# Optimization experiments

Measured on AMD Instinct MI355X. Metric: run time of the kernel, lower is better.

Reference implementation:

```python
import jax, jax.numpy as jnp
import numpy as np

B, NZ, L = 8, 16, 512
E, DM, NH, HD = 256, 512, 16, 32
FF, NL, E1D, PDIM, PMAX = 1024, 8, 32, 64, 24
EPS_LN = 1e-5
EPS_D = 1e-12


def _ln(x, g, b):
    m = jnp.mean(x, axis=-1, keepdims=True)
    v = jnp.mean((x - m) ** 2, axis=-1, keepdims=True)
    return (x - m) / jnp.sqrt(v + EPS_LN) * g + b


def setup_inputs() -> dict:
    key = jax.random.key(0)
    ks = iter(jax.random.split(key, 32))
    rn = lambda shape, fan: jax.random.normal(next(ks), shape, jnp.float32) / np.float32(np.sqrt(fan))
    inp = {
        "z": jax.random.normal(next(ks), (B, NZ, L), jnp.float32),
        "x": jax.random.uniform(next(ks), (B, 20, L), jnp.float32),
        # embeddings
        "pos_table": rn((2 * PMAX + 1, PDIM), 1.0),
        "aa_table": rn((20, E1D), 1.0),
        # embed_x: Linear(nz,E), relu, Linear(E,E)
        "ex_w1": rn((NZ, E), NZ), "ex_b1": jnp.zeros((E,), jnp.float32),
        "ex_w2": rn((E, E), E), "ex_b2": jnp.zeros((E,), jnp.float32),
        # per-layer stacked params
        "Wq": rn((NL, E, DM), E), "Wk": rn((NL, E, DM), E), "Wv": rn((NL, E, DM), E),
        "Wo": rn((NL, DM, E), DM), "bo": jnp.zeros((NL, E), jnp.float32),
        "W2d": rn((NL, PDIM, NH), PDIM), "b2d": jnp.zeros((NL, NH), jnp.float32),
        "W1": rn((NL, E + E1D, FF), E + E1D), "b1": jnp.zeros((NL, FF), jnp.float32),
        "W2": rn((NL, FF, E), FF), "b2": jnp.zeros((NL, E), jnp.float32),
        "g1": jnp.ones((NL, E), jnp.float32), "be1": jnp.zeros((NL, E), jnp.float32),
        "g2": jnp.ones((NL, E), jnp.float32), "be2": jnp.zeros((NL, E), jnp.float32),
        # mlp_3d: Linear(E,E), relu, Linear(E,3)
        "m3_w1": rn((E, E), E), "m3_b1": jnp.zeros((E,), jnp.float32),
        "m3_w2": rn((E, 3), E), "m3_b2": jnp.zeros((3,), jnp.float32),
    }
    return inp


def reference(z, x, pos_table, aa_table, ex_w1, ex_b1, ex_w2, ex_b2,
              Wq, Wk, Wv, Wo, bo, W2d, b2d, W1, b1, W2, b2,
              g1, be1, g2, be2, m3_w1, m3_b1, m3_w2, m3_b2):
    Bn, _, Ln = z.shape
    h = jnp.transpose(z, (0, 2, 1))  # (B, L, nz)
    # relative-position bins: argmin over integer bins == clip to [-PMAX, PMAX]
    rel = jnp.arange(Ln)[None, :] - jnp.arange(Ln)[:, None]
    bins = jnp.clip(rel, -PMAX, PMAX) + PMAX
    pe = pos_table[bins]  # (L, L, PDIM), batch-replicated
    e_aa = aa_table[jnp.argmax(x, axis=1)]  # (B, L, E1D)
    # embed_x MLP
    h = jax.nn.relu(h @ ex_w1 + ex_b1) @ ex_w2 + ex_b2  # (B, L, E)
    scale = np.float32(1.0 / np.sqrt(DM))  # dp_attn_norm='d_model'
    for i in range(NL):
        q = (h @ Wq[i]).reshape(Bn, Ln, NH, HD) * scale
        k = (h @ Wk[i]).reshape(Bn, Ln, NH, HD)
        v = (h @ Wv[i]).reshape(Bn, Ln, NH, HD)
        # learned pairwise bias: mlp_2d then transpose(1,3).transpose(2,3) -> bias[h,i,j] = out[i,j,h]
        bias = jnp.einsum('lmp,ph->hlm', pe, W2d[i]) + b2d[i][:, None, None]
        scores = jnp.einsum('blhd,bmhd->bhlm', q, k) + bias[None]
        attn = jax.nn.softmax(scores, axis=-1)
        o = jnp.einsum('bhlm,bmhd->blhd', attn, v).reshape(Bn, Ln, DM)
        h = _ln(h + (o @ Wo[i] + bo[i]), g1[i], be1[i])
        um = jnp.concatenate([h, e_aa], axis=-1)  # (B, L, E+E1D)
        s2 = jax.nn.relu(um @ W1[i] + b1[i]) @ W2[i] + b2[i]
        h = _ln(h + s2, g2[i], be2[i])
    r = jax.nn.relu(h @ m3_w1 + m3_b1) @ m3_w2 + m3_b2  # (B, L, 3)
    # distance map (get_coords=False path)
    d = jnp.sqrt(jnp.sum((r[:, None, :, :] - r[:, :, None, :]) ** 2, axis=-1) + EPS_D)
    return d  # (B, L, L)
```

## Files before the change

### kernel.cpp

```cpp
#include <hip/hip_runtime.h>
#include <math.h>

constexpr int Bn = 8, NZ = 16, Ln = 512;
constexpr int E = 256, DM = 512, NH = 16, HD = 32;
constexpr int FF = 1024, NL = 8, E1D = 32, PDIM = 64, PMAX = 24;
constexpr int ROWS = Bn * Ln;
constexpr float QSCALE = 0.04419417382415922f;

typedef __attribute__((ext_vector_type(8))) short bf16x8;
typedef __attribute__((ext_vector_type(4))) float floatx4;

__device__ inline unsigned short f2b(float f) {
  union { float f; unsigned u; } v; v.f = f;
  unsigned r = (v.u + 0x7FFF + ((v.u >> 16) & 1)) >> 16;
  return (unsigned short)r;
}
__device__ inline float b2f(unsigned short u) {
  union { unsigned u; float f; } v; v.u = ((unsigned)u) << 16; return v.f;
}

__device__ inline void gll16(const void* g, void* l) {
  __builtin_amdgcn_global_load_lds(
      (const __attribute__((address_space(1))) void*)g,
      (__attribute__((address_space(3))) void*)l, 16, 0, 0);
}

__global__ __launch_bounds__(256) void transpose_qkv(
    const float* __restrict__ Wq, const float* __restrict__ Wk,
    const float* __restrict__ Wv, unsigned short* __restrict__ qkvT)
{
  __shared__ float t[32][33];
  int zb = blockIdx.z;
  int which = zb / NL, l = zb % NL;
  const float* s = (which == 0 ? Wq : which == 1 ? Wk : Wv) + (size_t)l * E * DM;
  unsigned short* d = qkvT + (size_t)l * 3 * DM * E + (size_t)which * DM * E;
  int c0 = blockIdx.x * 32, r0 = blockIdx.y * 32;
  int tx = threadIdx.x & 31, ty = threadIdx.x >> 5;
  #pragma unroll
  for (int i = 0; i < 4; ++i)
    t[ty + i * 8][tx] = s[(size_t)(r0 + ty + i * 8) * DM + c0 + tx];
  __syncthreads();
  #pragma unroll
  for (int i = 0; i < 4; ++i)
    d[(size_t)(c0 + ty + i * 8) * E + r0 + tx] = f2b(t[tx][ty + i * 8]);
}

__global__ __launch_bounds__(256) void transpose_bf16(
    const float* __restrict__ src, unsigned short* __restrict__ dst,
    int R, int C, size_t sls, size_t dls)
{
  __shared__ float t[32][33];
  int l = blockIdx.z;
  int c0 = blockIdx.x * 32, r0 = blockIdx.y * 32;
  int tx = threadIdx.x & 31, ty = threadIdx.x >> 5;
  const float* s = src + (size_t)l * sls;
  unsigned short* d = dst + (size_t)l * dls;
  #pragma unroll
  for (int i = 0; i < 4; ++i)
    t[ty + i * 8][tx] = s[(size_t)(r0 + ty + i * 8) * C + c0 + tx];
  __syncthreads();
  #pragma unroll
  for (int i = 0; i < 4; ++i)
    d[(size_t)(c0 + ty + i * 8) * R + r0 + tx] = f2b(t[tx][ty + i * 8]);
}

__global__ __launch_bounds__(256) void embed1_kernel(
    const float* __restrict__ z, const float* __restrict__ x,
    const float* __restrict__ aa,
    const float* __restrict__ w1, const float* __restrict__ b1,
    float* __restrict__ t0, unsigned short* __restrict__ umb)
{
  int row = blockIdx.x;
  int b = row >> 9, l = row & (Ln - 1);
  int t = threadIdx.x;
  __shared__ float zs[NZ];
  __shared__ int am_s;
  if (t < NZ) zs[t] = z[((size_t)b * NZ + t) * Ln + l];
  if (t == 0) {
    const float* xp = x + (size_t)b * 20 * Ln + l;
    int am = 0; float bv = xp[0];
    for (int c = 1; c < 20; ++c) { float vv = xp[(size_t)c * Ln]; if (vv > bv) { bv = vv; am = c; } }
    am_s = am;
  }
  __syncthreads();
  float a1 = b1[t];
  #pragma unroll
  for (int nz = 0; nz < NZ; ++nz) a1 += zs[nz] * w1[nz * E + t];
  t0[(size_t)row * E + t] = fmaxf(a1, 0.f);
  if (t < E1D) umb[(size_t)row * (E + E1D) + E + t] = f2b(aa[am_s * E1D + t]);
}

__global__ __launch_bounds__(256) void bias_kernel(
    const float* __restrict__ pos, const float* __restrict__ W2d,
    const float* __restrict__ b2d, float* __restrict__ bias49)
{
  int layer = blockIdx.x;
  for (int idx = threadIdx.x; idx < NH * 49; idx += 256) {
    int hh = idx / 49, bin = idx % 49;
    float acc = b2d[layer * NH + hh];
    for (int p = 0; p < PDIM; ++p)
      acc += pos[bin * PDIM + p] * W2d[((size_t)layer * PDIM + p) * NH + hh];
    bias49[(size_t)layer * NH * 49 + hh * 49 + bin] = acc;
  }
}

template<int BM, int BN, bool BIAS, bool RELU, bool OUTBF16, bool QKV>
__global__ __launch_bounds__(256) void gemm_mfma(
    const unsigned short* __restrict__ A, const unsigned short* __restrict__ Bt,
    const float* __restrict__ bias,
    float* __restrict__ Cf, unsigned short* __restrict__ Cb, int N, int K)
{
  constexpr int MT = BM / 32, NT = BN / 32;
  __shared__ __align__(16) unsigned short As[BM][32];
  __shared__ __align__(16) unsigned short Bs[BN][32];
  const int tid = threadIdx.x;
  const int wave = tid >> 6, ln = tid & 63;
  const int quad = ln >> 4, l16 = ln & 15;
  const int wm = wave >> 1, wn = wave & 1;
  const int m0 = blockIdx.y * BM, n0 = blockIdx.x * BN;

  const int lrow = ln >> 2, chunk = ln & 3;
  const int schunk = chunk ^ ((lrow >> 1) & 3);
  const unsigned short* aSrc = A + (size_t)(m0 + wave * 16 + lrow) * K + schunk * 8;
  const unsigned short* bSrc = Bt + (size_t)(n0 + wave * 16 + lrow) * K + schunk * 8;
  const int rkey = (l16 >> 1) & 3;

  floatx4 acc[MT][NT] = {};

  for (int kb = 0; kb < K; kb += 32) {
    __syncthreads();
    #pragma unroll
    for (int it = 0; it < BM / 64; ++it)
      gll16(aSrc + (size_t)it * 64 * K + kb, &As[it * 64 + wave * 16][0]);
    #pragma unroll
    for (int it = 0; it < BN / 64; ++it)
      gll16(bSrc + (size_t)it * 64 * K + kb, &Bs[it * 64 + wave * 16][0]);
    __syncthreads();
    bf16x8 af[MT], bfr[NT];
    #pragma unroll
    for (int i = 0; i < MT; ++i)
      af[i] = *(const bf16x8*)&As[wm * (BM / 2) + i * 16 + l16][(quad ^ rkey) * 8];
    #pragma unroll
    for (int j = 0; j < NT; ++j)
      bfr[j] = *(const bf16x8*)&Bs[wn * (BN / 2) + j * 16 + l16][(quad ^ rkey) * 8];
    #pragma unroll
    for (int i = 0; i < MT; ++i)
      #pragma unroll
      for (int j = 0; j < NT; ++j)
        acc[i][j] = __builtin_amdgcn_mfma_f32_16x16x32_bf16(af[i], bfr[j], acc[i][j], 0, 0, 0);
  }

  #pragma unroll
  for (int i = 0; i < MT; ++i)
    #pragma unroll
    for (int j = 0; j < NT; ++j) {
      int col = n0 + wn * (BN / 2) + j * 16 + l16;
      float bv = BIAS ? bias[col] : 0.f;
      float sc = QKV ? (col < 512 ? QSCALE : 1.f) : 1.f;
      #pragma unroll
      for (int r = 0; r < 4; ++r) {
        int rowg = m0 + wm * (BM / 2) + i * 16 + quad * 4 + r;
        float v = acc[i][j][r] * sc + bv;
        if (RELU) v = fmaxf(v, 0.f);
        if (OUTBF16) Cb[(size_t)rowg * N + col] = f2b(v);
        else Cf[(size_t)rowg * N + col] = v;
      }
    }
}

__global__ __launch_bounds__(256) void gemm_n256(
    const unsigned short* __restrict__ A, const unsigned short* __restrict__ Bt,
    const float* __restrict__ bias, const float* __restrict__ resid,
    float* __restrict__ Cf, int K)
{
  __shared__ __align__(16) unsigned short As[32][64];
  __shared__ __align__(16) unsigned short Bs[32][64];
  const int tid = threadIdx.x;
  const int wave = tid >> 6, ln = tid & 63;
  const int quad = ln >> 4, l16 = ln & 15;
  const int wm = wave >> 1, wn = wave & 1;
  const int m0 = blockIdx.y * 32, n0 = blockIdx.x * 32;

  const int lrow = ln >> 3, chunk = ln & 7;
  const int schunk = chunk ^ lrow;
  const unsigned short* ap = A + (size_t)(m0 + wave * 8 + lrow) * K + schunk * 8;
  const unsigned short* bp = Bt + (size_t)(n0 + wave * 8 + lrow) * K + schunk * 8;
  const int rkey = l16 & 7;

  floatx4 acc = {};

  for (int kb = 0; kb < K; kb += 64) {
    __syncthreads();
    gll16(ap + kb, &As[wave * 8][0]);
    gll16(bp + kb, &Bs[wave * 8][0]);
    __syncthreads();
    #pragma unroll
    for (int kc = 0; kc < 2; ++kc) {
      bf16x8 af = *(const bf16x8*)&As[wm * 16 + l16][((kc * 4 + quad) ^ rkey) * 8];
      bf16x8 bf = *(const bf16x8*)&Bs[wn * 16 + l16][((kc * 4 + quad) ^ rkey) * 8];
      acc = __builtin_amdgcn_mfma_f32_16x16x32_bf16(af, bf, acc, 0, 0, 0);
    }
  }

  const int col = n0 + wn * 16 + l16;
  const float bv = bias[col];
  #pragma unroll
  for (int r = 0; r < 4; ++r) {
    int rowg = m0 + wm * 16 + quad * 4 + r;
    Cf[(size_t)rowg * 256 + col] = acc[r] + bv + resid[(size_t)rowg * 256 + col];
  }
}

__global__ __launch_bounds__(256) void attn_kernel(
    const unsigned short* __restrict__ qkv, const float* __restrict__ bias49,
    unsigned short* __restrict__ o)
{
  const int i0 = blockIdx.x * 64;
  const int bh = blockIdx.y;
  const int b = bh >> 4, hh = bh & 15;
  const int tid = threadIdx.x;
  const int wave = tid >> 6, ln = tid & 63;
  const int quad = ln >> 4, l16 = ln & 15;

  __shared__ __align__(16) unsigned short Kt[64][40];
  __shared__ __align__(16) unsigned short Vt[32][72];
  __shared__ __align__(16) unsigned short Pw[4][2][16][72];
  __shared__ float bsh[49];

  if (tid < 49) bsh[tid] = bias49[hh * 49 + tid];

  const unsigned short* qkvb = qkv + (size_t)b * Ln * 1536;

  const int qrow = i0 + wave * 16 + l16;
  const bf16x8 qf = *(const bf16x8*)(qkvb + (size_t)qrow * 1536 + hh * 32 + quad * 8);

  float m[4], l[4];
  #pragma unroll
  for (int r = 0; r < 4; ++r) { m[r] = -1e30f; l[r] = 0.f; }
  floatx4 acc_o[2] = {};

  const int krow = tid >> 2, kch = (tid & 3) * 8;
  const int vkey = tid & 63, vch = (tid >> 6) * 8;

  for (int jt = 0; jt < 8; ++jt) {
    const int j0 = jt * 64;
    __syncthreads();
    *(float4*)&Kt[krow][kch] =
        *(const float4*)(qkvb + (size_t)(j0 + krow) * 1536 + 512 + hh * 32 + kch);
    bf16x8 vv = *(const bf16x8*)(qkvb + (size_t)(j0 + vkey) * 1536 + 1024 + hh * 32 + vch);
    #pragma unroll
    for (int i = 0; i < 8; ++i) Vt[vch + i][vkey] = (unsigned short)vv[i];
    __syncthreads();

    floatx4 s4[4];
    #pragma unroll
    for (int t = 0; t < 4; ++t) {
      bf16x8 kf = *(const bf16x8*)&Kt[16 * t + l16][quad * 8];
      s4[t] = __builtin_amdgcn_mfma_f32_16x16x32_bf16(qf, kf, (floatx4){0.f, 0.f, 0.f, 0.f}, 0, 0, 0);
    }
    const int relmin = j0 - (i0 + 63), relmax = j0 + 63 - i0;
    if (relmin >= PMAX) {
      float bc = bsh[48];
      #pragma unroll
      for (int t = 0; t < 4; ++t)
        #pragma unroll
        for (int r = 0; r < 4; ++r) s4[t][r] += bc;
    } else if (relmax <= -PMAX) {
      float bc = bsh[0];
      #pragma unroll
      for (int t = 0; t < 4; ++t)
        #pragma unroll
        for (int r = 0; r < 4; ++r) s4[t][r] += bc;
    } else {
      const int base_rel = (j0 + l16) - (i0 + wave * 16 + quad * 4);
      #pragma unroll
      for (int t = 0; t < 4; ++t)
        #pragma unroll
        for (int r = 0; r < 4; ++r) {
          int rel = base_rel + 16 * t - r;
          rel = rel < -PMAX ? -PMAX : (rel > PMAX ? PMAX : rel);
          s4[t][r] += bsh[rel + PMAX];
        }
    }

    float mloc[4], alpha[4], psum[4];
    #pragma unroll
    for (int r = 0; r < 4; ++r) {
      mloc[r] = fmaxf(fmaxf(s4[0][r], s4[1][r]), fmaxf(s4[2][r], s4[3][r]));
      #pragma unroll
      for (int off = 1; off < 16; off <<= 1)
        mloc[r] = fmaxf(mloc[r], __shfl_xor(mloc[r], off, 64));
      float mnew = fmaxf(m[r], mloc[r]);
      alpha[r] = __expf(m[r] - mnew);
      m[r] = mnew;
      psum[r] = 0.f;
    }
    #pragma unroll
    for (int t = 0; t < 4; ++t)
      #pragma unroll
      for (int r = 0; r < 4; ++r) {
        float p = __expf(s4[t][r] - m[r]);
        s4[t][r] = p;
        psum[r] += p;
      }
    #pragma unroll
    for (int r = 0; r < 4; ++r) {
      #pragma unroll
      for (int off = 1; off < 16; off <<= 1)
        psum[r] += __shfl_xor(psum[r], off, 64);
      l[r] = l[r] * alpha[r] + psum[r];
      acc_o[0][r] *= alpha[r];
      acc_o[1][r] *= alpha[r];
    }

    #pragma unroll
    for (int t = 0; t < 4; ++t)
      #pragma unroll
      for (int r = 0; r < 4; ++r) {
        float p = s4[t][r];
        unsigned short hi = f2b(p);
        unsigned short lo = f2b(p - b2f(hi));
        Pw[wave][0][quad * 4 + r][16 * t + l16] = hi;
        Pw[wave][1][quad * 4 + r][16 * t + l16] = lo;
      }

    #pragma unroll
    for (int kh = 0; kh < 2; ++kh) {
      bf16x8 phi = *(const bf16x8*)&Pw[wave][0][l16][kh * 32 + quad * 8];
      bf16x8 plo = *(const bf16x8*)&Pw[wave][1][l16][kh * 32 + quad * 8];
      #pragma unroll
      for (int nt = 0; nt < 2; ++nt) {
        bf16x8 vf = *(const bf16x8*)&Vt[nt * 16 + l16][kh * 32 + quad * 8];
        acc_o[nt] = __builtin_amdgcn_mfma_f32_16x16x32_bf16(phi, vf, acc_o[nt], 0, 0, 0);
        acc_o[nt] = __builtin_amdgcn_mfma_f32_16x16x32_bf16(plo, vf, acc_o[nt], 0, 0, 0);
      }
    }
  }

  #pragma unroll
  for (int r = 0; r < 4; ++r) {
    float inv = 1.f / l[r];
    size_t rowg = (size_t)b * Ln + i0 + wave * 16 + quad * 4 + r;
    #pragma unroll
    for (int nt = 0; nt < 2; ++nt)
      o[rowg * 512 + hh * 32 + nt * 16 + l16] = f2b(acc_o[nt][r] * inv);
  }
}

__global__ __launch_bounds__(256) void ln_kernel(
    const float* __restrict__ xin, const float* __restrict__ g,
    const float* __restrict__ be, float* __restrict__ hout,
    unsigned short* __restrict__ bout, int bstride)
{
  const int w = threadIdx.x >> 6, lane = threadIdx.x & 63;
  const size_t row = (size_t)blockIdx.x * 4 + w;
  const int c0 = lane * 4;
  float4 v = *(const float4*)(xin + row * E + c0);
  float s = v.x + v.y + v.z + v.w;
  float s2 = v.x * v.x + v.y * v.y + v.z * v.z + v.w * v.w;
  #pragma unroll
  for (int off = 1; off < 64; off <<= 1) {
    s += __shfl_xor(s, off, 64);
    s2 += __shfl_xor(s2, off, 64);
  }
  const float mean = s * (1.f / E);
  const float rstd = rsqrtf(s2 * (1.f / E) - mean * mean + 1e-5f);
  const float4 gv = *(const float4*)(g + c0);
  const float4 bv = *(const float4*)(be + c0);
  float4 y;
  y.x = (v.x - mean) * rstd * gv.x + bv.x;
  y.y = (v.y - mean) * rstd * gv.y + bv.y;
  y.z = (v.z - mean) * rstd * gv.z + bv.z;
  y.w = (v.w - mean) * rstd * gv.w + bv.w;
  *(float4*)(hout + row * E + c0) = y;
  ushort4 yb;
  yb.x = f2b(y.x); yb.y = f2b(y.y); yb.z = f2b(y.z); yb.w = f2b(y.w);
  *(ushort4*)(bout + row * (size_t)bstride + c0) = yb;
}

template<bool RELU, bool BIAS, bool MIRROR>
__global__ __launch_bounds__(256) void gemm64f(
    const float* __restrict__ A, const float* __restrict__ B,
    const float* __restrict__ bias, float* __restrict__ C,
    unsigned short* __restrict__ mir, int N, int K)
{
  __shared__ __align__(16) float As[16][64];
  __shared__ __align__(16) float Bss[16][68];
  const int tid = threadIdx.x;
  const int tx = tid & 15, ty = tid >> 4;
  const int m0 = blockIdx.y * 64, n0 = blockIdx.x * 64;
  const int arow = tid >> 2, acol = (tid & 3) * 4;
  const int brow = tid >> 6, bcol = tid & 63;
  float acc[4][4] = {};
  for (int kb = 0; kb < K; kb += 16) {
    __syncthreads();
    float4 av = *(const float4*)(A + (size_t)(m0 + arow) * K + kb + acol);
    As[acol + 0][arow] = av.x; As[acol + 1][arow] = av.y;
    As[acol + 2][arow] = av.z; As[acol + 3][arow] = av.w;
    #pragma unroll
    for (int kk = 0; kk < 4; ++kk)
      Bss[brow + kk * 4][bcol] = B[(size_t)(kb + brow + kk * 4) * N + n0 + bcol];
    __syncthreads();
    #pragma unroll
    for (int k = 0; k < 16; ++k) {
      float4 a = *(const float4*)&As[k][4 * ty];
      float4 b = *(const float4*)&Bss[k][4 * tx];
      float av4[4] = {a.x, a.y, a.z, a.w};
      float bv4[4] = {b.x, b.y, b.z, b.w};
      #pragma unroll
      for (int ii = 0; ii < 4; ++ii)
        #pragma unroll
        for (int jj = 0; jj < 4; ++jj)
          acc[ii][jj] += av4[ii] * bv4[jj];
    }
  }
  #pragma unroll
  for (int ii = 0; ii < 4; ++ii) {
    size_t row = (size_t)m0 + 4 * ty + ii;
    int col = n0 + 4 * tx;
    float4 vv;
    vv.x = acc[ii][0]; vv.y = acc[ii][1]; vv.z = acc[ii][2]; vv.w = acc[ii][3];
    if (BIAS) {
      float4 bb = *(const float4*)(bias + col);
      vv.x += bb.x; vv.y += bb.y; vv.z += bb.z; vv.w += bb.w;
    }
    if (RELU) {
      vv.x = fmaxf(vv.x, 0.f); vv.y = fmaxf(vv.y, 0.f);
      vv.z = fmaxf(vv.z, 0.f); vv.w = fmaxf(vv.w, 0.f);
    }
    *(float4*)(C + row * N + col) = vv;
    if (MIRROR) {
      ushort4 mv;
      mv.x = f2b(vv.x); mv.y = f2b(vv.y); mv.z = f2b(vv.z); mv.w = f2b(vv.w);
      *(ushort4*)(mir + row * N + col) = mv;
    }
  }
}

__global__ __launch_bounds__(256) void final_r_kernel(
    const float* __restrict__ t1, const float* __restrict__ w2,
    const float* __restrict__ b2, float* __restrict__ r)
{
  int row = blockIdx.x, t = threadIdx.x;
  float xv = t1[(size_t)row * E + t];
  float p0 = xv * w2[t * 3 + 0];
  float p1 = xv * w2[t * 3 + 1];
  float p2 = xv * w2[t * 3 + 2];
  #pragma unroll
  for (int off = 32; off > 0; off >>= 1) {
    p0 += __shfl_down(p0, off, 64);
    p1 += __shfl_down(p1, off, 64);
    p2 += __shfl_down(p2, off, 64);
  }
  __shared__ float red[4][3];
  if ((t & 63) == 0) { int w = t >> 6; red[w][0] = p0; red[w][1] = p1; red[w][2] = p2; }
  __syncthreads();
  if (t < 3)
    r[(size_t)row * 3 + t] = red[0][t] + red[1][t] + red[2][t] + red[3][t] + b2[t];
}

__global__ __launch_bounds__(512) void dist_kernel(
    const float* __restrict__ r, float* __restrict__ out)
{
  int bi = blockIdx.x;
  int j = threadIdx.x;
  int b = bi >> 9;
  float x0 = r[(size_t)bi * 3 + 0];
  float y0 = r[(size_t)bi * 3 + 1];
  float z0 = r[(size_t)bi * 3 + 2];
  const float* rj = r + ((size_t)b * Ln + j) * 3;
  float dx = rj[0] - x0, dy = rj[1] - y0, dz = rj[2] - z0;
  out[(size_t)bi * Ln + j] = sqrtf(dx * dx + dy * dy + dz * dz + 1e-12f);
}

extern "C" void kernel_launch(void* const* d_in, const int* in_sizes, int n_in,
                              void* d_out, int out_size, void* d_ws, size_t ws_size,
                              hipStream_t stream)
{
  const float* z     = (const float*)d_in[0];
  const float* x     = (const float*)d_in[1];
  const float* pos   = (const float*)d_in[2];
  const float* aa    = (const float*)d_in[3];
  const float* ex_w1 = (const float*)d_in[4];
  const float* ex_b1 = (const float*)d_in[5];
  const float* ex_w2 = (const float*)d_in[6];
  const float* ex_b2 = (const float*)d_in[7];
  const float* Wq    = (const float*)d_in[8];
  const float* Wk    = (const float*)d_in[9];
  const float* Wv    = (const float*)d_in[10];
  const float* Wo    = (const float*)d_in[11];
  const float* bo    = (const float*)d_in[12];
  const float* W2d   = (const float*)d_in[13];
  const float* b2d   = (const float*)d_in[14];
  const float* W1    = (const float*)d_in[15];
  const float* b1    = (const float*)d_in[16];
  const float* W2    = (const float*)d_in[17];
  const float* b2    = (const float*)d_in[18];
  const float* g1    = (const float*)d_in[19];
  const float* be1   = (const float*)d_in[20];
  const float* g2    = (const float*)d_in[21];
  const float* be2   = (const float*)d_in[22];
  const float* m3w1  = (const float*)d_in[23];
  const float* m3b1  = (const float*)d_in[24];
  const float* m3w2  = (const float*)d_in[25];
  const float* m3b2  = (const float*)d_in[26];

  float* ws     = (float*)d_ws;
  float* h      = ws;
  float* t0     = h + (size_t)ROWS * E;
  float* r      = t0 + (size_t)ROWS * E;
  float* bias49 = r + (size_t)ROWS * 3;
  unsigned short* us = (unsigned short*)(bias49 + NL * NH * 49);
  unsigned short* hb   = us;
  unsigned short* umb  = hb  + (size_t)ROWS * E;
  unsigned short* qkvb = umb + (size_t)ROWS * (E + E1D);
  unsigned short* ob   = qkvb + (size_t)ROWS * 3 * DM;
  unsigned short* t1b  = ob  + (size_t)ROWS * DM;
  unsigned short* qkvT = t1b + (size_t)ROWS * FF;
  unsigned short* WoT  = qkvT + (size_t)NL * 3 * DM * E;
  unsigned short* W1T  = WoT  + (size_t)NL * E * DM;
  unsigned short* W2T  = W1T  + (size_t)NL * FF * (E+E1D);
  float* tmp = t0;
  float* t1f = (float*)t1b;

  transpose_qkv<<<dim3(DM/32, E/32, 3*NL), 256, 0, stream>>>(Wq, Wk, Wv, qkvT);
  transpose_bf16<<<dim3(E/32, DM/32, NL), 256, 0, stream>>>(
      Wo, WoT, DM, E, (size_t)DM * E, (size_t)DM * E);
  transpose_bf16<<<dim3(FF/32, (E+E1D)/32, NL), 256, 0, stream>>>(
      W1, W1T, E + E1D, FF, (size_t)(E+E1D) * FF, (size_t)(E+E1D) * FF);
  transpose_bf16<<<dim3(E/32, FF/32, NL), 256, 0, stream>>>(
      W2, W2T, FF, E, (size_t)FF * E, (size_t)FF * E);

  embed1_kernel<<<ROWS, 256, 0, stream>>>(z, x, aa, ex_w1, ex_b1, t0, umb);
  gemm64f<false,true,true><<<dim3(E/64, ROWS/64), 256, 0, stream>>>(
      t0, ex_w2, ex_b2, h, hb, E, E);
  bias_kernel<<<NL, 256, 0, stream>>>(pos, W2d, b2d, bias49);

  for (int i = 0; i < NL; ++i) {
    gemm_mfma<64,128,false,false,true,true><<<dim3(12, 64), 256, 0, stream>>>(
        hb, qkvT + (size_t)i * 3 * DM * E, nullptr, nullptr, qkvb, 3 * DM, E);
    attn_kernel<<<dim3(Ln/64, Bn*NH), 256, 0, stream>>>(
        qkvb, bias49 + (size_t)i * NH * 49, ob);
    gemm_n256<<<dim3(E/32, ROWS/32), 256, 0, stream>>>(
        ob, WoT + (size_t)i * DM * E, bo + (size_t)i * E, h, tmp, DM);
    ln_kernel<<<ROWS/4, 256, 0, stream>>>(tmp, g1 + (size_t)i * E, be1 + (size_t)i * E, h, umb, E + E1D);
    gemm_mfma<64,64,true,true,true,false><<<dim3(FF/64, ROWS/64), 256, 0, stream>>>(
        umb, W1T + (size_t)i * FF * (E+E1D), b1 + (size_t)i * FF, nullptr, t1b, FF, E + E1D);
    gemm_n256<<<dim3(E/32, ROWS/32), 256, 0, stream>>>(
        t1b, W2T + (size_t)i * E * FF, b2 + (size_t)i * E, h, tmp, FF);
    ln_kernel<<<ROWS/4, 256, 0, stream>>>(tmp, g2 + (size_t)i * E, be2 + (size_t)i * E, h, hb, E);
  }

  gemm64f<true,true,false><<<dim3(E/64, ROWS/64), 256, 0, stream>>>(
      h, m3w1, m3b1, t1f, nullptr, E, E);
  final_r_kernel<<<ROWS, 256, 0, stream>>>(t1f, m3w2, m3b2, r);
  dist_kernel<<<ROWS, 512, 0, stream>>>(r, (float*)d_out);
}
```

Before: 841.9 us.

## Fuse output-projection GEMMs with residual LayerNorm and use BK=64 for QKV

Replaces the N=256 GEMM plus separate LayerNorm kernel pair with a single gemm_ln kernel. Each block computes a full 16x256 row tile, adds bias and residual in shared memory, and applies LayerNorm before writing fp32 h and the bf16 copy. This removes a launch and an fp32 intermediate round-trip per LN, but each block now reloads the whole 256-column weight slice and the grid shrinks to 256 blocks. The QKV GEMM also gets a BK=64 K-loop variant to halve the barrier count per K step.

New measurement: 822.8 us. 1.02x faster.

```diff
diff --git a/kernel.cpp b/kernel.cpp
--- a/kernel.cpp
+++ b/kernel.cpp
@@ -104,50 +104,83 @@
   }
 }
 
-template<int BM, int BN, bool BIAS, bool RELU, bool OUTBF16, bool QKV>
+template<int BM, int BN, int BK, bool BIAS, bool RELU, bool OUTBF16, bool QKV>
 __global__ __launch_bounds__(256) void gemm_mfma(
     const unsigned short* __restrict__ A, const unsigned short* __restrict__ Bt,
     const float* __restrict__ bias,
     float* __restrict__ Cf, unsigned short* __restrict__ Cb, int N, int K)
 {
   constexpr int MT = BM / 32, NT = BN / 32;
-  __shared__ __align__(16) unsigned short As[BM][32];
-  __shared__ __align__(16) unsigned short Bs[BN][32];
+  __shared__ __align__(16) unsigned short As[BM][BK];
+  __shared__ __align__(16) unsigned short Bs[BN][BK];
   const int tid = threadIdx.x;
   const int wave = tid >> 6, ln = tid & 63;
   const int quad = ln >> 4, l16 = ln & 15;
   const int wm = wave >> 1, wn = wave & 1;
   const int m0 = blockIdx.y * BM, n0 = blockIdx.x * BN;
 
-  const int lrow = ln >> 2, chunk = ln & 3;
-  const int schunk = chunk ^ ((lrow >> 1) & 3);
-  const unsigned short* aSrc = A + (size_t)(m0 + wave * 16 + lrow) * K + schunk * 8;
-  const unsigned short* bSrc = Bt + (size_t)(n0 + wave * 16 + lrow) * K + schunk * 8;
-  const int rkey = (l16 >> 1) & 3;
-
   floatx4 acc[MT][NT] = {};
 
-  for (int kb = 0; kb < K; kb += 32) {
-    __syncthreads();
-    #pragma unroll
-    for (int it = 0; it < BM / 64; ++it)
-      gll16(aSrc + (size_t)it * 64 * K + kb, &As[it * 64 + wave * 16][0]);
-    #pragma unroll
-    for (int it = 0; it < BN / 64; ++it)
-      gll16(bSrc + (size_t)it * 64 * K + kb, &Bs[it * 64 + wave * 16][0]);
-    __syncthreads();
-    bf16x8 af[MT], bfr[NT];
-    #pragma unroll
-    for (int i = 0; i < MT; ++i)
-      af[i] = *(const bf16x8*)&As[wm * (BM / 2) + i * 16 + l16][(quad ^ rkey) * 8];
-    #pragma unroll
-    for (int j = 0; j < NT; ++j)
-      bfr[j] = *(const bf16x8*)&Bs[wn * (BN / 2) + j * 16 + l16][(quad ^ rkey) * 8];
-    #pragma unroll
-    for (int i = 0; i < MT; ++i)
+  if constexpr (BK == 32) {
+    const int lrow = ln >> 2, chunk = ln & 3;
+    const int schunk = chunk ^ ((lrow >> 1) & 3);
+    const unsigned short* aSrc = A + (size_t)(m0 + wave * 16 + lrow) * K + schunk * 8;
+    const unsigned short* bSrc = Bt + (size_t)(n0 + wave * 16 + lrow) * K + schunk * 8;
+    const int rkey = (l16 >> 1) & 3;
+
+    for (int kb = 0; kb < K; kb += 32) {
+      __syncthreads();
+      #pragma unroll
+      for (int it = 0; it < BM / 64; ++it)
+        gll16(aSrc + (size_t)it * 64 * K + kb, &As[it * 64 + wave * 16][0]);
+      #pragma unroll
+      for (int it = 0; it < BN / 64; ++it)
+        gll16(bSrc + (size_t)it * 64 * K + kb, &Bs[it * 64 + wave * 16][0]);
+      __syncthreads();
+      bf16x8 af[MT], bfr[NT];
+      #pragma unroll
+      for (int i = 0; i < MT; ++i)
+        af[i] = *(const bf16x8*)&As[wm * (BM / 2) + i * 16 + l16][(quad ^ rkey) * 8];
       #pragma unroll
       for (int j = 0; j < NT; ++j)
-        acc[i][j] = __builtin_amdgcn_mfma_f32_16x16x32_bf16(af[i], bfr[j], acc[i][j], 0, 0, 0);
+        bfr[j] = *(const bf16x8*)&Bs[wn * (BN / 2) + j * 16 + l16][(quad ^ rkey) * 8];
+      #pragma unroll
+      for (int i = 0; i < MT; ++i)
+        #pragma unroll
+        for (int j = 0; j < NT; ++j)
+          acc[i][j] = __builtin_amdgcn_mfma_f32_16x16x32_bf16(af[i], bfr[j], acc[i][j], 0, 0, 0);
+    }
+  } else {
+    const int lrow = ln >> 3, chunk = ln & 7;
+    const int schunk = chunk ^ lrow;
+    const unsigned short* aSrc = A + (size_t)(m0 + wave * 8 + lrow) * K + schunk * 8;
+    const unsigned short* bSrc = Bt + (size_t)(n0 + wave * 8 + lrow) * K + schunk * 8;
+
+    for (int kb = 0; kb < K; kb += 64) {
+      __syncthreads();
+      #pragma unroll
+      for (int it = 0; it < BM / 32; ++it)
+        gll16(aSrc + (size_t)(it * 32) * K + kb, &As[it * 32 + wave * 8][0]);
+      #pragma unroll
+      for (int it = 0; it < BN / 32; ++it)
+        gll16(bSrc + (size_t)(it * 32) * K + kb, &Bs[it * 32 + wave * 8][0]);
+      __syncthreads();
+      #pragma unroll
+      for (int kc = 0; kc < 2; ++kc) {
+        bf16x8 af[MT], bfr[NT];
+        #pragma unroll
+        for (int i = 0; i < MT; ++i)
+          af[i] = *(const bf16x8*)&As[wm * (BM / 2) + i * 16 + l16][(((kc * 4 + quad) ^ (l16 & 7)) * 8)];
+        #pragma unroll
+        for (int j = 0; j < NT; ++j)
+          bfr[j] = *(const bf16x8*)&Bs[wn * (BN / 2) + j * 16 + l16][(((kc * 4 + quad) ^ (l16 & 7)) * 8)];
+        #pragma unroll
+        for (int i = 0; i < MT; ++i)
+          #pragma unroll
+          for (int j = 0; j < NT; ++j)
+            acc[i][j] = __builtin_amdgcn_mfma_f32_16x16x32_bf16(af[i], bfr[j], acc[i][j], 0, 0, 0);
+      }
+    }
   }
 
   #pragma unroll
@@ -168,46 +201,82 @@
     }
 }
 
-__global__ __launch_bounds__(256) void gemm_n256(
+__global__ __launch_bounds__(256) void gemm_ln(
     const unsigned short* __restrict__ A, const unsigned short* __restrict__ Bt,
-    const float* __restrict__ bias, const float* __restrict__ resid,
-    float* __restrict__ Cf, int K)
-{
-  __shared__ __align__(16) unsigned short As[32][64];
-  __shared__ __align__(16) unsigned short Bs[32][64];
+    const float* __restrict__ bias, float* __restrict__ h,
+    const float* __restrict__ g, const float* __restrict__ be,
+    unsigned short* __restrict__ outb, int bstride, int K)
+{
+  __shared__ __align__(16) unsigned short As[16][64];
+  __shared__ __align__(16) unsigned short Bs[256][64];
+  __shared__ __align__(16) float vtile[16][260];
   const int tid = threadIdx.x;
-  const int wave = tid >> 6, ln = tid & 63;
+  const int w = tid >> 6, ln = tid & 63;
   const int quad = ln >> 4, l16 = ln & 15;
-  const int wm = wave >> 1, wn = wave & 1;
-  const int m0 = blockIdx.y * 32, n0 = blockIdx.x * 32;
-
+  const int m0 = blockIdx.x * 16;
   const int lrow = ln >> 3, chunk = ln & 7;
   const int schunk = chunk ^ lrow;
-  const unsigned short* ap = A + (size_t)(m0 + wave * 8 + lrow) * K + schunk * 8;
-  const unsigned short* bp = Bt + (size_t)(n0 + wave * 8 + lrow) * K + schunk * 8;
-  const int rkey = l16 & 7;
-
-  floatx4 acc = {};
+  const unsigned short* aSrc = A + (size_t)(m0 + w * 8 + lrow) * K + schunk * 8;
+  const unsigned short* bSrc = Bt + (size_t)(w * 8 + lrow) * K + schunk * 8;
+
+  floatx4 acc[4] = {};
 
   for (int kb = 0; kb < K; kb += 64) {
     __syncthreads();
-    gll16(ap + kb, &As[wave * 8][0]);
-    gll16(bp + kb, &Bs[wave * 8][0]);
+    if (w < 2) gll16(aSrc + kb, &As[w * 8][0]);
+    #pragma unroll
+    for (int it = 0; it < 8; ++it)
+      gll16(bSrc + (size_t)(it * 32) * K + kb, &Bs[it * 32 + w * 8][0]);
     __syncthreads();
     #pragma unroll
     for (int kc = 0; kc < 2; ++kc) {
-      bf16x8 af = *(const bf16x8*)&As[wm * 16 + l16][((kc * 4 + quad) ^ rkey) * 8];
-      bf16x8 bf = *(const bf16x8*)&Bs[wn * 16 + l16][((kc * 4 + quad) ^ rkey) * 8];
-      acc = __builtin_amdgcn_mfma_f32_16x16x32_bf16(af, bf, acc, 0, 0, 0);
-    }
-  }
-
-  const int col = n0 + wn * 16 + l16;
-  const float bv = bias[col];
-  #pragma unroll
-  for (int r = 0; r < 4; ++r) {
-    int rowg = m0 + wm * 16 + quad * 4 + r;
-    Cf[(size_t)rowg * 256 + col] = acc[r] + bv + resid[(size_t)rowg * 256 + col];
+      bf16x8 af = *(const bf16x8*)&As[l16][(((kc * 4 + quad) ^ (l16 & 7)) * 8)];
+      #pragma unroll
+      for (int nt = 0; nt < 4; ++nt) {
+        bf16x8 bf = *(const bf16x8*)&Bs[w * 64 + nt * 16 + l16][(((kc * 4 + quad) ^ (l16 & 7)) * 8)];
+        acc[nt] = __builtin_amdgcn_mfma_f32_16x16x32_bf16(af, bf, acc[nt], 0, 0, 0);
+      }
+    }
+  }
+
+  #pragma unroll
+  for (int nt = 0; nt < 4; ++nt) {
+    int col = w * 64 + nt * 16 + l16;
+    float bv = bias[col];
+    #pragma unroll
+    for (int r = 0; r < 4; ++r) {
+      int row = quad * 4 + r;
+      vtile[row][col] = acc[nt][r] + bv + h[(size_t)(m0 + row) * E + col];
+    }
+  }
+  __syncthreads();
+
+  const int c0 = ln * 4;
+  #pragma unroll
+  for (int rr = 0; rr < 4; ++rr) {
+    const int lr = w * 4 + rr;
+    float4 v = *(const float4*)&vtile[lr][c0];
+    float s = v.x + v.y + v.z + v.w;
+    float s2 = v.x * v.x + v.y * v.y + v.z * v.z + v.w * v.w;
+    #pragma unroll
+    for (int off = 1; off < 64; off <<= 1) {
+      s += __shfl_xor(s, off, 64);
+      s2 += __shfl_xor(s2, off, 64);
+    }
+    const float mean = s * (1.f / E);
+    const float rstd = rsqrtf(s2 * (1.f / E) - mean * mean + 1e-5f);
+    const float4 gv = *(const float4*)(g + c0);
+    const float4 bv = *(const float4*)(be + c0);
+    float4 y;
+    y.x = (v.x - mean) * rstd * gv.x + bv.x;
+    y.y = (v.y - mean) * rstd * gv.y + bv.y;
+    y.z = (v.z - mean) * rstd * gv.z + bv.z;
+    y.w = (v.w - mean) * rstd * gv.w + bv.w;
+    const size_t row = (size_t)(m0 + lr);
+    *(float4*)(h + row * E + c0) = y;
+    ushort4 yb;
+    yb.x = f2b(y.x); yb.y = f2b(y.y); yb.z = f2b(y.z); yb.w = f2b(y.w);
+    *(ushort4*)(outb + row * (size_t)bstride + c0) = yb;
   }
 }
 
@@ -345,37 +414,6 @@
     for (int nt = 0; nt < 2; ++nt)
       o[rowg * 512 + hh * 32 + nt * 16 + l16] = f2b(acc_o[nt][r] * inv);
   }
-}
-
-__global__ __launch_bounds__(256) void ln_kernel(
-    const float* __restrict__ xin, const float* __restrict__ g,
-    const float* __restrict__ be, float* __restrict__ hout,
-    unsigned short* __restrict__ bout, int bstride)
-{
-  const int w = threadIdx.x >> 6, lane = threadIdx.x & 63;
-  const size_t row = (size_t)blockIdx.x * 4 + w;
-  const int c0 = lane * 4;
-  float4 v = *(const float4*)(xin + row * E + c0);
-  float s = v.x + v.y + v.z + v.w;
-  float s2 = v.x * v.x + v.y * v.y + v.z * v.z + v.w * v.w;
-  #pragma unroll
-  for (int off = 1; off < 64; off <<= 1) {
-    s += __shfl_xor(s, off, 64);
-    s2 += __shfl_xor(s2, off, 64);
-  }
-  const float mean = s * (1.f / E);
-  const float rstd = rsqrtf(s2 * (1.f / E) - mean * mean + 1e-5f);
-  const float4 gv = *(const float4*)(g + c0);
-  const float4 bv = *(const float4*)(be + c0);
-  float4 y;
-  y.x = (v.x - mean) * rstd * gv.x + bv.x;
-  y.y = (v.y - mean) * rstd * gv.y + bv.y;
-  y.z = (v.z - mean) * rstd * gv.z + bv.z;
-  y.w = (v.w - mean) * rstd * gv.w + bv.w;
-  *(float4*)(hout + row * E + c0) = y;
-  ushort4 yb;
-  yb.x = f2b(y.x); yb.y = f2b(y.y); yb.z = f2b(y.z); yb.w = f2b(y.w);
-  *(ushort4*)(bout + row * (size_t)bstride + c0) = yb;
 }
 
 template<bool RELU, bool BIAS, bool MIRROR>
@@ -520,7 +558,6 @@
   unsigned short* WoT  = qkvT + (size_t)NL * 3 * DM * E;
   unsigned short* W1T  = WoT  + (size_t)NL * E * DM;
   unsigned short* W2T  = W1T  + (size_t)NL * FF * (E+E1D);
-  float* tmp = t0;
   float* t1f = (float*)t1b;
 
   transpose_qkv<<<dim3(DM/32, E/32, 3*NL), 256, 0, stream>>>(Wq, Wk, Wv, qkvT);
@@ -537,18 +574,18 @@
   bias_kernel<<<NL, 256, 0, stream>>>(pos, W2d, b2d, bias49);
 
   for (int i = 0; i < NL; ++i) {
-    gemm_mfma<64,128,false,false,true,true><<<dim3(12, 64), 256, 0, stream>>>(
+    gemm_mfma<64,128,64,false,false,true,true><<<dim3(12, 64), 256, 0, stream>>>(
         hb, qkvT + (size_t)i * 3 * DM * E, nullptr, nullptr, qkvb, 3 * DM, E);
     attn_kernel<<<dim3(Ln/64, Bn*NH), 256, 0, stream>>>(
         qkvb, bias49 + (size_t)i * NH * 49, ob);
-    gemm_n256<<<dim3(E/32, ROWS/32), 256, 0, stream>>>(
-        ob, WoT + (size_t)i * DM * E, bo + (size_t)i * E, h, tmp, DM);
-    ln_kernel<<<ROWS/4, 256, 0, stream>>>(tmp, g1 + (size_t)i * E, be1 + (size_t)i * E, h, umb, E + E1D);
-    gemm_mfma<64,64,true,true,true,false><<<dim3(FF/64, ROWS/64), 256, 0, stream>>>(
+    gemm_ln<<<ROWS/16, 256, 0, stream>>>(
+        ob, WoT + (size_t)i * DM * E, bo + (size_t)i * E, h,
+        g1 + (size_t)i * E, be1 + (size_t)i * E, umb, E + E1D, DM);
+    gemm_mfma<64,64,32,true,true,true,false><<<dim3(FF/64, ROWS/64), 256, 0, stream>>>(
         umb, W1T + (size_t)i * FF * (E+E1D), b1 + (size_t)i * FF, nullptr, t1b, FF, E + E1D);
-    gemm_n256<<<dim3(E/32, ROWS/32), 256, 0, stream>>>(
-        t1b, W2T + (size_t)i * E * FF, b2 + (size_t)i * E, h, tmp, FF);
-    ln_kernel<<<ROWS/4, 256, 0, stream>>>(tmp, g2 + (size_t)i * E, be2 + (size_t)i * E, h, hb, E);
+    gemm_ln<<<ROWS/16, 256, 0, stream>>>(
+        t1b, W2T + (size_t)i * E * FF, b2 + (size_t)i * E, h,
+        g2 + (size_t)i * E, be2 + (size_t)i * E, hb, E, FF);
   }
 
   gemm64f<true,true,false><<<dim3(E/64, ROWS/64), 256, 0, stream>>>(
```
